# Kernel tuning notes

Measured on AMD Instinct MI355X. Metric: run time of the kernel, lower is better.

The kernel has to match this reference:

```python
import jax, jax.numpy as jnp
import numpy as np
import math

N_EMBED = 1024
N_HEAD = 16
BLOCK_SIZE = 2048

def setup_inputs() -> dict:
    key = jax.random.key(0)
    k1, k2, k3, k4, k5 = jax.random.split(key, 5)
    s = 0.02
    x = jax.random.normal(k1, (2, 2048, N_EMBED), dtype=jnp.float32)
    W_qkv = jax.random.normal(k2, (N_EMBED, 3 * N_EMBED), dtype=jnp.float32) * s
    b_qkv = jax.random.normal(k3, (3 * N_EMBED,), dtype=jnp.float32) * s
    W_out = jax.random.normal(k4, (N_EMBED, N_EMBED), dtype=jnp.float32) * s
    b_out = jax.random.normal(k5, (N_EMBED,), dtype=jnp.float32) * s
    return {"x": x, "W_qkv": W_qkv, "b_qkv": b_qkv, "W_out": W_out, "b_out": b_out}

def reference(x, W_qkv, b_qkv, W_out, b_out):
    b, s, d = x.shape
    hd = d // N_HEAD  # head dim
    qkv = x @ W_qkv + b_qkv                       # [b, s, 3d]
    q, k, v = jnp.split(qkv, 3, axis=-1)
    # [b, h, s, hd]
    q = q.reshape(b, s, N_HEAD, hd).transpose(0, 2, 1, 3)
    k = k.reshape(b, s, N_HEAD, hd).transpose(0, 2, 1, 3)
    v = v.reshape(b, s, N_HEAD, hd).transpose(0, 2, 1, 3)
    scale = 1.0 / math.sqrt(hd)
    sims = jnp.einsum('bhqd,bhkd->bhqk', q, k) * scale  # [b, h, s, s]
    causal = jnp.tril(jnp.ones((s, s), dtype=bool))
    sims = jnp.where(causal[None, None], sims, -jnp.inf)
    probs = jax.nn.softmax(sims, axis=-1)
    attn = jnp.einsum('bhqk,bhkd->bhqd', probs, v)       # [b, h, s, hd]
    attn = attn.transpose(0, 2, 1, 3).reshape(b, s, d)
    return attn @ W_out + b_out
```

## Files before the change

kernel.cpp:

```cpp
#include <hip/hip_runtime.h>
#include <hip/hip_bf16.h>

typedef __attribute__((ext_vector_type(8))) short short8;
typedef __attribute__((ext_vector_type(4))) short short4v;
typedef __attribute__((ext_vector_type(4))) float f32x4;
typedef __attribute__((ext_vector_type(16))) float f32x16;
typedef __attribute__((ext_vector_type(4))) unsigned int u32x4;
typedef unsigned short u16;

__device__ __forceinline__ u16 f2bf(float f) {
  __hip_bfloat16 h = __float2bfloat16(f);
  return __builtin_bit_cast(unsigned short, h);
}

__device__ __forceinline__ unsigned pack2(float lo, float hi) {
  return (unsigned)f2bf(lo) | ((unsigned)f2bf(hi) << 16);
}

__device__ __forceinline__ void gload16(const u16* g, u16* l) {
  __builtin_amdgcn_global_load_lds(
      (const __attribute__((address_space(1))) unsigned int*)g,
      (__attribute__((address_space(3))) unsigned int*)l, 16, 0, 0);
}

__global__ void cvt_x_kernel(const float* __restrict__ in, u16* __restrict__ out, int n) {
  int i = (blockIdx.x * blockDim.x + threadIdx.x) * 4;
  if (i >= n) return;
  float4 f = *(const float4*)(in + i);
  uint2 pk;
  pk.x = pack2(f.x, f.y);
  pk.y = pack2(f.z, f.w);
  *(uint2*)(out + i) = pk;
}

__global__ void tcvt_kernel(const float* __restrict__ in, u16* __restrict__ out, int N) {
  __shared__ float tile[32][33];
  int n0 = blockIdx.x * 32, k0 = blockIdx.y * 32;
  int tx = threadIdx.x, ty = threadIdx.y;
#pragma unroll
  for (int r = 0; r < 4; ++r) {
    int k = ty + r * 8;
    tile[k][tx] = in[(size_t)(k0 + k) * N + n0 + tx];
  }
  __syncthreads();
#pragma unroll
  for (int r = 0; r < 4; ++r) {
    int n = ty + r * 8;
    out[(size_t)(n0 + n) * 1024 + k0 + tx] = f2bf(tile[tx][n]);
  }
}

template <int EPI>
__global__ __launch_bounds__(256, 2) void gemm_kernel(const u16* __restrict__ A,
                                                      const u16* __restrict__ Bt,
                                                      const float* __restrict__ bias,
                                                      void* __restrict__ outp) {
  __shared__ u16 Al[128 * 64];
  __shared__ u16 Bl[128 * 64];
  const int tid = threadIdx.x;
  const int lane = tid & 63, wid = tid >> 6;
  const int l15 = lane & 15, lg = lane >> 4;
  const int wm = wid >> 1, wn = wid & 1;
  const int m0 = blockIdx.y * 128, n0 = blockIdx.x * 128;

  f32x4 acc[4][4] = {};

  for (int k0 = 0; k0 < 1024; k0 += 64) {
    __syncthreads();
#pragma unroll
    for (int i = 0; i < 4; ++i) {
      int p = i * 4096 + tid * 16;
      int row = p >> 7;
      int lslot = ((p >> 4) & 7) ^ (row & 7);
      gload16(A + (size_t)(m0 + row) * 1024 + k0 + lslot * 8, Al + i * 2048 + wid * 512);
      gload16(Bt + (size_t)(n0 + row) * 1024 + k0 + lslot * 8, Bl + i * 2048 + wid * 512);
    }
    __syncthreads();
#pragma unroll
    for (int ks = 0; ks < 2; ++ks) {
      short8 af[4], bfr[4];
#pragma unroll
      for (int m = 0; m < 4; ++m) {
        int row = wm * 64 + m * 16 + l15;
        af[m] = *(const short8*)((const char*)Al + row * 128 + (((ks * 4 + lg) ^ (row & 7)) << 4));
      }
#pragma unroll
      for (int n = 0; n < 4; ++n) {
        int row = wn * 64 + n * 16 + l15;
        bfr[n] = *(const short8*)((const char*)Bl + row * 128 + (((ks * 4 + lg) ^ (row & 7)) << 4));
      }
#pragma unroll
      for (int m = 0; m < 4; ++m)
#pragma unroll
        for (int n = 0; n < 4; ++n)
          acc[m][n] = __builtin_amdgcn_mfma_f32_16x16x32_bf16(af[m], bfr[n], acc[m][n], 0, 0, 0);
    }
  }

  if (EPI == 0) {
    u16* qkv = (u16*)outp;
#pragma unroll
    for (int m = 0; m < 4; ++m)
#pragma unroll
      for (int n = 0; n < 4; ++n) {
        const int gcol = n0 + wn * 64 + n * 16 + l15;
        const int which = gcol >> 10, dd = gcol & 1023;
        const int h = dd >> 6, hd = dd & 63;
        const float bb = bias[gcol];
        const int grow0 = m0 + wm * 64 + m * 16 + lg * 4;
        const int b = grow0 >> 11, s0 = grow0 & 2047;
        if (which == 2) {
          short4v pk;
#pragma unroll
          for (int j = 0; j < 4; ++j) pk[j] = (short)f2bf(acc[m][n][j] + bb);
          *(short4v*)(qkv + (size_t)2 * 4194304 + ((size_t)(b * 16 + h) * 64 + hd) * 2048 + s0) = pk;
        } else {
          const float sc = (which == 0) ? 0.18033688011112042f : 1.0f;
#pragma unroll
          for (int j = 0; j < 4; ++j) {
            float v = (acc[m][n][j] + bb) * sc;
            qkv[(size_t)which * 4194304 + ((size_t)(b * 16 + h) * 2048 + s0 + j) * 64 + hd] = f2bf(v);
          }
        }
      }
  } else {
    float* O = (float*)outp;
#pragma unroll
    for (int m = 0; m < 4; ++m)
#pragma unroll
      for (int n = 0; n < 4; ++n) {
        const int gcol = n0 + wn * 64 + n * 16 + l15;
        const float bb = bias[gcol];
#pragma unroll
        for (int j = 0; j < 4; ++j) {
          const int grow = m0 + wm * 64 + m * 16 + lg * 4 + j;
          O[(size_t)grow * 1024 + gcol] = acc[m][n][j] + bb;
        }
      }
  }
}

__global__ __launch_bounds__(256, 2) void attn_kernel(const u16* __restrict__ Q,
                                                      const u16* __restrict__ K,
                                                      const u16* __restrict__ VT,
                                                      u16* __restrict__ Aout) {
  const int bh = blockIdx.y;
  const int p = blockIdx.x;
  const int tid = threadIdx.x, lane = tid & 63, wid = tid >> 6;
  const int l31 = lane & 31, h = lane >> 5;
  const int qs = wid & 1, kp = wid >> 1;

  __shared__ __align__(16) char smem[36864];
  u16(*Kl)[4096] = (u16(*)[4096])smem;
  u16(*Vl)[4096] = (u16(*)[4096])(smem + 16384);

  const u16* Qb = Q + (size_t)bh * 2048 * 64;
  const u16* Kb = K + (size_t)bh * 2048 * 64;
  const u16* Vb = VT + (size_t)bh * 64 * 2048;

  const int qA = p * 64 + qs * 32;
  const int qB = (31 - p) * 64 + qs * 32;
  const int R = 32 - p;

  short8 qfA[4], qfB[4];
#pragma unroll
  for (int ks = 0; ks < 4; ++ks) {
    qfA[ks] = *(const short8*)(Qb + (size_t)(qA + l31) * 64 + ks * 16 + h * 8);
    qfB[ks] = *(const short8*)(Qb + (size_t)(qB + l31) * 64 + ks * 16 + h * 8);
  }

  f32x16 accA[2] = {}, accB[2] = {};
  float mA = -1e30f, mB = -1e30f, lA = 0.f, lB = 0.f;

  auto stage = [&](int buf, size_t kb) {
#pragma unroll
    for (int i = 0; i < 2; ++i) {
      const int row = i * 32 + (tid >> 3);
      const int sc = ((tid & 7) ^ (row & 7)) * 8;
      gload16(Kb + (kb + row) * 64 + sc, &Kl[buf][i * 2048 + wid * 512]);
      gload16(Vb + (size_t)row * 2048 + kb + sc, &Vl[buf][i * 2048 + wid * 512]);
    }
  };

  stage(0, 0);
  __syncthreads();

  for (int t = 0; t < R; ++t) {
    const int cur = t & 1;
    if (t + 1 < R) stage(cur ^ 1, (size_t)(t + 1) * 64);

    const int kvbase = t * 64 + kp * 32;
    const bool actB = kvbase <= qB + 31;
    const bool actA = kvbase <= qA + 31;
    if (actB) {
      short8 kf[4];
      const int krow = kp * 32 + l31;
#pragma unroll
      for (int ks = 0; ks < 4; ++ks)
        kf[ks] = *(const short8*)((const char*)&Kl[cur][0] + krow * 128 +
                                  (((ks * 2 + h) ^ (krow & 7)) << 4));
      short8 vf[2][2];
#pragma unroll
      for (int n = 0; n < 2; ++n) {
        const int row = n * 32 + l31;
        const int rx = row & 7;
        const char* base = (const char*)&Vl[cur][0] + row * 128;
#pragma unroll
        for (int ks = 0; ks < 2; ++ks) {
          const int cb = kp * 32 + ks * 16 + 4 * h;
          const int c2 = cb + 8;
          const short4v lo = *(const short4v*)(base + (((cb >> 3) ^ rx) << 4) + ((cb & 4) << 1));
          const short4v hi = *(const short4v*)(base + (((c2 >> 3) ^ rx) << 4) + ((c2 & 4) << 1));
          vf[n][ks] = (short8){lo[0], lo[1], lo[2], lo[3], hi[0], hi[1], hi[2], hi[3]};
        }
      }

      auto strip = [&](const short8(&qf)[4], f32x16(&acc)[2], float& m, float& l, int q0) {
        f32x16 sa = {};
        __builtin_amdgcn_s_setprio(1);
#pragma unroll
        for (int ks = 0; ks < 4; ++ks)
          sa = __builtin_amdgcn_mfma_f32_32x32x16_bf16(kf[ks], qf[ks], sa, 0, 0, 0);
        __builtin_amdgcn_s_setprio(0);
        if (kvbase == q0) {
#pragma unroll
          for (int r = 0; r < 16; ++r) {
            const int kvr = (r & 3) + 8 * (r >> 2) + 4 * h;
            if (kvr > l31) sa[r] = -1e30f;
          }
        }
        const float t0 = fmaxf(fmaxf(sa[0], sa[1]), sa[2]);
        const float t1 = fmaxf(fmaxf(sa[3], sa[4]), sa[5]);
        const float t2 = fmaxf(fmaxf(sa[6], sa[7]), sa[8]);
        const float t3 = fmaxf(fmaxf(sa[9], sa[10]), sa[11]);
        const float t4 = fmaxf(fmaxf(sa[12], sa[13]), sa[14]);
        float rm = fmaxf(fmaxf(fmaxf(t0, t1), t2), fmaxf(fmaxf(t3, t4), sa[15]));
        rm = fmaxf(rm, __shfl_xor(rm, 32));
        if (!__all(rm <= m + 5.0f)) {
          const float mn = fmaxf(m, rm);
          const float corr = exp2f(m - mn);
          m = mn;
          l *= corr;
#pragma unroll
          for (int n = 0; n < 2; ++n)
#pragma unroll
            for (int r = 0; r < 16; ++r) acc[n][r] *= corr;
        }
#pragma unroll
        for (int r = 0; r < 16; ++r) sa[r] = exp2f(sa[r] - m);
        float rs = (((sa[0] + sa[1]) + (sa[2] + sa[3])) + ((sa[4] + sa[5]) + (sa[6] + sa[7]))) +
                   (((sa[8] + sa[9]) + (sa[10] + sa[11])) + ((sa[12] + sa[13]) + (sa[14] + sa[15])));
        l += rs + __shfl_xor(rs, 32);
        unsigned c[8];
#pragma unroll
        for (int i = 0; i < 8; ++i) c[i] = pack2(sa[2 * i], sa[2 * i + 1]);
        const short8 pk0 = __builtin_bit_cast(short8, (u32x4){c[0], c[1], c[2], c[3]});
        const short8 pk1 = __builtin_bit_cast(short8, (u32x4){c[4], c[5], c[6], c[7]});
        __builtin_amdgcn_s_setprio(1);
#pragma unroll
        for (int n = 0; n < 2; ++n) {
          acc[n] = __builtin_amdgcn_mfma_f32_32x32x16_bf16(vf[n][0], pk0, acc[n], 0, 0, 0);
          acc[n] = __builtin_amdgcn_mfma_f32_32x32x16_bf16(vf[n][1], pk1, acc[n], 0, 0, 0);
        }
        __builtin_amdgcn_s_setprio(0);
      };

      strip(qfB, accB, mB, lB, qB);
      if (actA) strip(qfA, accA, mA, lA, qA);
    }
    __syncthreads();
  }

  float* comb = (float*)smem;
  float* pA = comb + ((qs * 2 + 0) * 64 + lane) * 36;
  float* pB = comb + ((qs * 2 + 1) * 64 + lane) * 36;
  if (kp == 1) {
    pA[0] = mA; pA[1] = lA;
    pB[0] = mB; pB[1] = lB;
#pragma unroll
    for (int n = 0; n < 2; ++n)
#pragma unroll
      for (int r = 0; r < 16; ++r) {
        pA[2 + n * 16 + r] = accA[n][r];
        pB[2 + n * 16 + r] = accB[n][r];
      }
  }
  __syncthreads();
  if (kp == 0) {
    const int b = bh >> 4, hh = bh & 15;
    auto merge_store = [&](const float* pp, const f32x16(&acc)[2], float m0, float l0, int q0) {
      const float m1 = pp[0], l1 = pp[1];
      const float mn = fmaxf(m0, m1);
      const float c0 = exp2f(m0 - mn), c1 = exp2f(m1 - mn);
      const float inv = 1.0f / (l0 * c0 + l1 * c1);
      u16* rowp = Aout + (size_t)(b * 2048 + q0 + l31) * 1024 + hh * 64;
#pragma unroll
      for (int n = 0; n < 2; ++n)
#pragma unroll
        for (int r = 0; r < 16; r += 2) {
          const int hd = n * 32 + (r & 3) + 8 * (r >> 2) + 4 * h;
          const float v0 = (acc[n][r] * c0 + pp[2 + n * 16 + r] * c1) * inv;
          const float v1 = (acc[n][r + 1] * c0 + pp[2 + n * 16 + r + 1] * c1) * inv;
          *(unsigned*)(rowp + hd) = pack2(v0, v1);
        }
    };
    merge_store(pA, accA, mA, lA, qA);
    merge_store(pB, accB, mB, lB, qB);
  }
}

extern "C" void kernel_launch(void* const* d_in, const int* in_sizes, int n_in,
                              void* d_out, int out_size, void* d_ws, size_t ws_size,
                              hipStream_t stream) {
  const float* x = (const float*)d_in[0];
  const float* Wqkv = (const float*)d_in[1];
  const float* bqkv = (const float*)d_in[2];
  const float* Wout = (const float*)d_in[3];
  const float* bout = (const float*)d_in[4];

  char* ws = (char*)d_ws;
  u16* Xb = (u16*)(ws + 0);
  u16* WqkvT = (u16*)(ws + 8388608);
  u16* WoutT = (u16*)(ws + 14680064);
  u16* QKV = (u16*)(ws + 16777216);
  u16* Attn = Xb;

  cvt_x_kernel<<<4096, 256, 0, stream>>>(x, Xb, 4194304);
  tcvt_kernel<<<dim3(96, 32), dim3(32, 8), 0, stream>>>(Wqkv, WqkvT, 3072);
  tcvt_kernel<<<dim3(32, 32), dim3(32, 8), 0, stream>>>(Wout, WoutT, 1024);
  gemm_kernel<0><<<dim3(24, 32), 256, 0, stream>>>(Xb, WqkvT, bqkv, QKV);
  attn_kernel<<<dim3(16, 32), 256, 0, stream>>>(QKV, QKV + 4194304, QKV + 8388608, Attn);
  gemm_kernel<1><<<dim3(8, 32), 256, 0, stream>>>(Attn, WoutT, bout, d_out);
}
```

Baseline: 112.2 us.

## Permute V sequence layout for single-load fragments and batch QK MFMAs across strips

The QKV epilogue now writes V with a permuted order of 4-element sequence groups, so each attention V fragment can be fetched from LDS as one 16-byte read instead of two 8-byte reads plus a shuffle. The QK^T MFMAs for both query strips are also issued back to back before either strip's softmax, which gives the scheduler more independent matrix work to overlap with the exponentials. The cost is a coupled layout contract between the projection kernel and the attention kernel, and two score accumulators held live at once, which raises register pressure.

New measurement: 110.4 us. About the same (-1.6%).

```diff
diff --git a/kernel.cpp b/kernel.cpp
--- a/kernel.cpp
+++ b/kernel.cpp
@@ -110,10 +110,13 @@
         const int grow0 = m0 + wm * 64 + m * 16 + lg * 4;
         const int b = grow0 >> 11, s0 = grow0 & 2047;
         if (which == 2) {
+          const int bsub = (s0 >> 2) & 3;
+          const int bper = (bsub == 1) ? 2 : (bsub == 2) ? 1 : bsub;
+          const int s0p = (s0 & ~15) | (bper << 2);
           short4v pk;
 #pragma unroll
           for (int j = 0; j < 4; ++j) pk[j] = (short)f2bf(acc[m][n][j] + bb);
-          *(short4v*)(qkv + (size_t)2 * 4194304 + ((size_t)(b * 16 + h) * 64 + hd) * 2048 + s0) = pk;
+          *(short4v*)(qkv + (size_t)2 * 4194304 + ((size_t)(b * 16 + h) * 64 + hd) * 2048 + s0p) = pk;
         } else {
           const float sc = (which == 0) ? 0.18033688011112042f : 1.0f;
 #pragma unroll
@@ -193,35 +196,34 @@
     const bool actB = kvbase <= qB + 31;
     const bool actA = kvbase <= qA + 31;
     if (actB) {
-      short8 kf[4];
+      short8 kf[4], vf[2][2];
       const int krow = kp * 32 + l31;
 #pragma unroll
       for (int ks = 0; ks < 4; ++ks)
         kf[ks] = *(const short8*)((const char*)&Kl[cur][0] + krow * 128 +
                                   (((ks * 2 + h) ^ (krow & 7)) << 4));
-      short8 vf[2][2];
-#pragma unroll
-      for (int n = 0; n < 2; ++n) {
-        const int row = n * 32 + l31;
-        const int rx = row & 7;
-        const char* base = (const char*)&Vl[cur][0] + row * 128;
+#pragma unroll
+      for (int n = 0; n < 2; ++n)
 #pragma unroll
         for (int ks = 0; ks < 2; ++ks) {
-          const int cb = kp * 32 + ks * 16 + 4 * h;
-          const int c2 = cb + 8;
-          const short4v lo = *(const short4v*)(base + (((cb >> 3) ^ rx) << 4) + ((cb & 4) << 1));
-          const short4v hi = *(const short4v*)(base + (((c2 >> 3) ^ rx) << 4) + ((c2 & 4) << 1));
-          vf[n][ks] = (short8){lo[0], lo[1], lo[2], lo[3], hi[0], hi[1], hi[2], hi[3]};
-        }
-      }
-
-      auto strip = [&](const short8(&qf)[4], f32x16(&acc)[2], float& m, float& l, int q0) {
-        f32x16 sa = {};
-        __builtin_amdgcn_s_setprio(1);
+          const int row = n * 32 + l31;
+          vf[n][ks] = *(const short8*)((const char*)&Vl[cur][0] + row * 128 +
+                                       (((kp * 4 + ks * 2 + h) ^ (row & 7)) << 4));
+        }
+
+      f32x16 saB = {}, saA = {};
+      __builtin_amdgcn_s_setprio(1);
+#pragma unroll
+      for (int ks = 0; ks < 4; ++ks)
+        saB = __builtin_amdgcn_mfma_f32_32x32x16_bf16(kf[ks], qfB[ks], saB, 0, 0, 0);
+      if (actA) {
 #pragma unroll
         for (int ks = 0; ks < 4; ++ks)
-          sa = __builtin_amdgcn_mfma_f32_32x32x16_bf16(kf[ks], qf[ks], sa, 0, 0, 0);
-        __builtin_amdgcn_s_setprio(0);
+          saA = __builtin_amdgcn_mfma_f32_32x32x16_bf16(kf[ks], qfA[ks], saA, 0, 0, 0);
+      }
+      __builtin_amdgcn_s_setprio(0);
+
+      auto finish = [&](f32x16& sa, f32x16(&acc)[2], float& m, float& l, int q0) {
         if (kvbase == q0) {
 #pragma unroll
           for (int r = 0; r < 16; ++r) {
@@ -265,8 +267,8 @@
         __builtin_amdgcn_s_setprio(0);
       };
 
-      strip(qfB, accB, mB, lB, qB);
-      if (actA) strip(qfA, accA, mA, lA, qA);
+      finish(saB, accB, mB, lB, qB);
+      if (actA) finish(saA, accA, mA, lA, qA);
     }
     __syncthreads();
   }
```
